# Kernel tuning notes

Measured on AMD Instinct MI355X. Metric: run time of the kernel, lower is better.

The kernel has to match this reference:

```python
import jax, jax.numpy as jnp
import numpy as np

N_NODES = 50000
N_EDGES = 800000
D_IN = 128
HIDDEN = 128
NUM_GRAPHS = 64
NUM_CLASSES = 6


def setup_inputs() -> dict:
    key = jax.random.key(0)
    ks = jax.random.split(key, 12)
    x = jax.random.normal(ks[0], (N_NODES, D_IN), dtype=jnp.float32)
    edge_index = jax.random.randint(ks[1], (2, N_EDGES), 0, N_NODES, dtype=jnp.int64)
    batch = jnp.sort(jax.random.randint(ks[2], (N_NODES,), 0, NUM_GRAPHS, dtype=jnp.int64))
    def glorot(k, fan_in, fan_out):
        s = jnp.sqrt(6.0 / (fan_in + fan_out)).astype(jnp.float32)
        return jax.random.uniform(k, (fan_in, fan_out), jnp.float32, -s, s)
    W0 = glorot(ks[3], D_IN, HIDDEN)
    b0 = jnp.zeros((HIDDEN,), jnp.float32)
    W1 = glorot(ks[4], HIDDEN, HIDDEN)
    b1 = jnp.zeros((HIDDEN,), jnp.float32)
    W2 = glorot(ks[5], HIDDEN, HIDDEN)
    b2 = jnp.zeros((HIDDEN,), jnp.float32)
    lin_W = glorot(ks[6], HIDDEN, NUM_CLASSES)
    lin_b = jnp.zeros((NUM_CLASSES,), jnp.float32)
    return {"x": x, "edge_index": edge_index, "batch": batch,
            "W0": W0, "b0": b0, "W1": W1, "b1": b1, "W2": W2, "b2": b2,
            "lin_W": lin_W, "lin_b": lin_b}


def reference(x, edge_index, batch, W0, b0, W1, b1, W2, b2, lin_W, lin_b):
    # GCNConv (PyG default): add self-loops, symmetric degree norm,
    # out = scatter_add(norm * (xW)[src] -> dst) + bias, then ReLU.
    loop = jnp.arange(N_NODES, dtype=edge_index.dtype)
    src = jnp.concatenate([edge_index[0], loop])  # message sources (x_j)
    dst = jnp.concatenate([edge_index[1], loop])  # aggregation targets
    deg = jax.ops.segment_sum(jnp.ones_like(dst, x.dtype), dst, num_segments=N_NODES)
    dinv = jnp.where(deg > 0, jax.lax.rsqrt(deg), 0.0)
    norm = (dinv[src] * dinv[dst])[:, None]  # [E+N, 1]

    h = x
    for W, b in ((W0, b0), (W1, b1), (W2, b2)):
        hw = h @ W                                   # [N, H] dense projection
        agg = jax.ops.segment_sum(hw[src] * norm, dst, num_segments=N_NODES)
        h = jax.nn.relu(agg + b)

    # global_mean_pool over graph ids
    counts = jax.ops.segment_sum(jnp.ones((N_NODES,), x.dtype), batch, num_segments=NUM_GRAPHS)
    embedding = jax.ops.segment_sum(h, batch, num_segments=NUM_GRAPHS) / jnp.maximum(counts, 1.0)[:, None]
    # dropout is identity in eval mode
    logits = embedding @ lin_W + lin_b
    return logits, embedding
```

## Files before the change

### kernel.cpp

```cpp
#include <hip/hip_runtime.h>

#define N_NODES 50000
#define HIDDEN 128
#define NUM_GRAPHS 64
#define NUM_CLASSES 6
#define SLOT_SHIFT 6
#define NB 392
#define BUCKET_CAP 3072
#define P1_CHUNK 2048
#define CONV_BLOCKS 192
#define LSTR 136

typedef __attribute__((ext_vector_type(8))) short short8;
typedef __attribute__((ext_vector_type(4))) float float4v;
typedef __attribute__((ext_vector_type(2))) float float2v;

__device__ __forceinline__ unsigned short f2b(float f) {
    unsigned u = __float_as_uint(f);
    return (unsigned short)((u + 0x7FFFu + ((u >> 16) & 1u)) >> 16);
}
__device__ __forceinline__ unsigned char f2e4m3(float f) {
    return (unsigned char)(__builtin_amdgcn_cvt_pk_fp8_f32(f, f, 0, false) & 0xFF);
}

__global__ __launch_bounds__(256) void pass1(const float* __restrict__ W0, const float* __restrict__ W1,
                                             const float* __restrict__ W2, unsigned short* __restrict__ wb,
                                             const int* __restrict__ src, const int* __restrict__ dst,
                                             int* __restrict__ gcursor, unsigned* __restrict__ ebuf, int e) {
    if (blockIdx.x < CONV_BLOCKS) {
        int i = blockIdx.x * 256 + threadIdx.x;
        int wsel = i >> 14;
        int r = i & 16383;
        int j = r & 7;
        int lane = (r >> 3) & 63;
        int f = r >> 9;
        int ki = f >> 3, nt = f & 7;
        int k = ki * 32 + (lane >> 4) * 8 + j;
        int c = nt * 16 + (lane & 15);
        const float* W = (wsel == 0) ? W0 : ((wsel == 1) ? W1 : W2);
        wb[i] = f2b(W[k * 128 + c]);
        return;
    }
    __shared__ unsigned hist[NB];
    __shared__ unsigned base[NB];
    const int t = threadIdx.x;
    const int start = (blockIdx.x - CONV_BLOCKS) * P1_CHUNK;
    for (int i = t; i < NB; i += 256) hist[i] = 0;
    __syncthreads();
    int lb[8];
    unsigned pk[8], lr[8];
#pragma unroll
    for (int k = 0; k < 8; k++) {
        int i = start + k * 256 + t;
        lb[k] = -1;
        if (i < e) {
            int d = dst[i];
            int s = src[i];
            lb[k] = d >> 7;
            pk[k] = ((unsigned)(d & 127) << 16) | (unsigned)s;
            lr[k] = atomicAdd(&hist[lb[k]], 1u);
        }
    }
    __syncthreads();
    for (int b = t; b < NB; b += 256)
        base[b] = (unsigned)atomicAdd(&gcursor[b], (int)hist[b]);
    __syncthreads();
#pragma unroll
    for (int k = 0; k < 8; k++) {
        if (lb[k] >= 0) {
            unsigned pos = base[lb[k]] + lr[k];
            if (pos < BUCKET_CAP) ebuf[lb[k] * BUCKET_CAP + pos] = pk[k];
        }
    }
}

__global__ __launch_bounds__(256) void pass2(const unsigned* __restrict__ ebuf, const int* __restrict__ gcursor,
                                             const float* __restrict__ x,
                                             unsigned short* __restrict__ csr16, int* __restrict__ cntc,
                                             float* __restrict__ dinv, unsigned char* __restrict__ xs8, int n) {
    __shared__ unsigned short csr_lds[128 * 64];
    __shared__ unsigned cnt[128];
    const int b = blockIdx.x;
    const int t = threadIdx.x;
    if (t < 128) {
        cnt[t] = 0;
        csr_lds[t * 64] = (unsigned short)(b * 128 + t);
    }
    __syncthreads();
    const int nb = min(gcursor[b], BUCKET_CAP);
    for (int i = t; i < nb; i += 256) {
        unsigned e = ebuf[b * BUCKET_CAP + i];
        int dl = (int)(e >> 16);
        unsigned r = atomicAdd(&cnt[dl], 1u);
        if (r < 63) csr_lds[dl * 64 + 1 + r] = (unsigned short)(e & 0xFFFFu);
    }
    __syncthreads();
    {
        const unsigned* cu = (const unsigned*)csr_lds;
        unsigned* gout = (unsigned*)(csr16 + (size_t)b * 8192);
#pragma unroll
        for (int it = 0; it < 16; it++) gout[it * 256 + t] = cu[it * 256 + t];
    }
    if (t < 128) {
        int node = b * 128 + t;
        if (node < n) {
            int deg1 = (int)cnt[t] + 1;
            cntc[node] = min(deg1, 64);
            dinv[node] = rsqrtf((float)deg1);
        }
    }
#pragma unroll
    for (int it = 0; it < 16; it++) {
        int idx = it * 256 + t;
        int nl = idx >> 5;
        int el = (idx & 31) * 4;
        int gnode = b * 128 + nl;
        if (gnode < n) {
            float sc = rsqrtf((float)((int)cnt[nl] + 1));
            float4 v = *(const float4*)&x[gnode * 128 + el];
            unsigned lo = __builtin_amdgcn_cvt_pk_fp8_f32(v.x * sc, v.y * sc, 0, false);
            unsigned pkd = __builtin_amdgcn_cvt_pk_fp8_f32(v.z * sc, v.w * sc, lo, true);
            *(unsigned*)&xs8[gnode * 128 + el] = pkd;
        }
    }
}

__global__ __launch_bounds__(256) void fused_layer(const unsigned char* __restrict__ hs8,
                                                   const int* __restrict__ cntc,
                                                   const unsigned short* __restrict__ csr16,
                                                   const float* __restrict__ dinv,
                                                   const unsigned short* __restrict__ wb,
                                                   const float* __restrict__ bias,
                                                   const float* __restrict__ rowscale,
                                                   unsigned char* __restrict__ hout8,
                                                   const int* __restrict__ batchp,
                                                   float* __restrict__ embp) {
    __shared__ __align__(16) unsigned short tlds[16 * LSTR];
    __shared__ int bsh[16];
    const int wave = threadIdx.x >> 6;
    const int lane = threadIdx.x & 63;
    const int grp = lane >> 4;
    const int fl = lane & 15;
    const int node0 = blockIdx.x * 16;
    const int base_node = node0 + wave * 4;

    int nbv[4], mycv[4];
#pragma unroll
    for (int i = 0; i < 4; i++) nbv[i] = cntc[base_node + i];
#pragma unroll
    for (int i = 0; i < 4; i++)
        mycv[i] = (lane < nbv[i]) ? (int)csr16[((base_node + i) << SLOT_SHIFT) + lane] : 0;

    for (int i = 0; i < 4; i++) {
        const int node = base_node + i;
        const int nb = nbv[i];
        const int nbm1 = nb - 1;
        float acc[8];
#pragma unroll
        for (int j = 0; j < 8; j++) acc[j] = 0.f;
        int myc = mycv[i];
        for (int c0 = 0; c0 < nb; c0 += 32) {
            int cc[8];
            float m[8];
#pragma unroll
            for (int k = 0; k < 8; k++) {
                int e = c0 + k * 4 + grp;
                m[k] = (e < nb) ? 1.f : 0.f;
                cc[k] = __shfl(myc, min(e, nbm1), 64);
            }
            uint2 u[8];
#pragma unroll
            for (int k = 0; k < 8; k++)
                u[k] = *(const uint2*)&hs8[cc[k] * 128 + fl * 8];
#pragma unroll
            for (int k = 0; k < 8; k++) {
                float2v f01 = __builtin_amdgcn_cvt_pk_f32_fp8(u[k].x, false);
                float2v f23 = __builtin_amdgcn_cvt_pk_f32_fp8(u[k].x, true);
                float2v f45 = __builtin_amdgcn_cvt_pk_f32_fp8(u[k].y, false);
                float2v f67 = __builtin_amdgcn_cvt_pk_f32_fp8(u[k].y, true);
                acc[0] += m[k] * f01.x;  acc[1] += m[k] * f01.y;
                acc[2] += m[k] * f23.x;  acc[3] += m[k] * f23.y;
                acc[4] += m[k] * f45.x;  acc[5] += m[k] * f45.y;
                acc[6] += m[k] * f67.x;  acc[7] += m[k] * f67.y;
            }
        }
#pragma unroll
        for (int j = 0; j < 8; j++) {
            acc[j] += __shfl_xor(acc[j], 16, 64);
            acc[j] += __shfl_xor(acc[j], 32, 64);
        }
        if (grp == 0) {
            const float dv = dinv[node];
            short8 o;
#pragma unroll
            for (int j = 0; j < 8; j++) o[j] = (short)f2b(acc[j] * dv);
            *(short8*)&tlds[(wave * 4 + i) * LSTR + fl * 8] = o;
        }
    }
    if (embp && threadIdx.x < 16) bsh[threadIdx.x] = batchp[node0 + threadIdx.x];
    __syncthreads();

    const int m = fl;
    const int quad = grp;
    const int nt0 = wave * 2;
    const short* B = (const short*)wb;
    float4v acc2[2];
    acc2[0] = (float4v){0.f, 0.f, 0.f, 0.f};
    acc2[1] = (float4v){0.f, 0.f, 0.f, 0.f};
#pragma unroll
    for (int ki = 0; ki < 4; ki++) {
        short8 a = *(const short8*)&tlds[m * LSTR + ki * 32 + quad * 8];
#pragma unroll
        for (int q = 0; q < 2; q++) {
            short8 b = *(const short8*)&B[((ki * 8 + nt0 + q) * 64 + lane) * 8];
            acc2[q] = __builtin_amdgcn_mfma_f32_16x16x32_bf16(a, b, acc2[q], 0, 0, 0);
        }
    }

    if (!embp) {
        float sc[4];
#pragma unroll
        for (int reg = 0; reg < 4; reg++) {
            int row = node0 + quad * 4 + reg;
            sc[reg] = rowscale[row];
        }
#pragma unroll
        for (int q = 0; q < 2; q++) {
            int c = (nt0 + q) * 16 + m;
            float bv = bias[c];
#pragma unroll
            for (int reg = 0; reg < 4; reg++) {
                int row = node0 + quad * 4 + reg;
                float v = fmaxf(acc2[q][reg] + bv, 0.f) * sc[reg];
                hout8[row * 128 + c] = f2e4m3(v);
            }
        }
    } else {
        const int g0 = bsh[0], g15 = bsh[15];
#pragma unroll
        for (int q = 0; q < 2; q++) {
            int c = (nt0 + q) * 16 + m;
            float bv = bias[c];
            float v0 = fmaxf(acc2[q][0] + bv, 0.f);
            float v1 = fmaxf(acc2[q][1] + bv, 0.f);
            float v2 = fmaxf(acc2[q][2] + bv, 0.f);
            float v3 = fmaxf(acc2[q][3] + bv, 0.f);
            if (g0 == g15) {
                float s = v0 + v1 + v2 + v3;
                s += __shfl_xor(s, 16, 64);
                s += __shfl_xor(s, 32, 64);
                if (quad == 0) atomicAdd(&embp[g0 * HIDDEN + c], s);
            } else {
                for (int gg = g0; gg <= g15; ++gg) {
                    float s = (bsh[quad * 4 + 0] == gg ? v0 : 0.f)
                            + (bsh[quad * 4 + 1] == gg ? v1 : 0.f)
                            + (bsh[quad * 4 + 2] == gg ? v2 : 0.f)
                            + (bsh[quad * 4 + 3] == gg ? v3 : 0.f);
                    s += __shfl_xor(s, 16, 64);
                    s += __shfl_xor(s, 32, 64);
                    if (quad == 0) atomicAdd(&embp[gg * HIDDEN + c], s);
                }
            }
        }
    }
}

__global__ __launch_bounds__(128) void finalize_kernel(const float* __restrict__ emb,
                                                       const int* __restrict__ batch,
                                                       const float* __restrict__ linW, const float* __restrict__ linb,
                                                       float* out, int n) {
    const int g = blockIdx.x;
    const int f = threadIdx.x;
    __shared__ float es[128];
    __shared__ int bnd[2];
    if (f < 2) {
        int target = g + f;
        int lo = 0, hi = n;
        while (lo < hi) {
            int mid = (lo + hi) >> 1;
            if (batch[mid] < target) lo = mid + 1; else hi = mid;
        }
        bnd[f] = lo;
    }
    __syncthreads();
    float c = (float)max(bnd[1] - bnd[0], 1);
    float e = emb[g * HIDDEN + f] / c;
    out[NUM_GRAPHS * NUM_CLASSES + g * HIDDEN + f] = e;
    es[f] = e;
    __syncthreads();
    if (f < NUM_CLASSES) {
        float s = linb[f];
        for (int k = 0; k < HIDDEN; k++) s += es[k] * linW[k * NUM_CLASSES + f];
        out[g * NUM_CLASSES + f] = s;
    }
}

extern "C" void kernel_launch(void* const* d_in, const int* in_sizes, int n_in,
                              void* d_out, int out_size, void* d_ws, size_t ws_size,
                              hipStream_t stream) {
    const float* x    = (const float*)d_in[0];
    const int*   ei   = (const int*)d_in[1];
    const int*   batch= (const int*)d_in[2];
    const float* W0   = (const float*)d_in[3];
    const float* b0   = (const float*)d_in[4];
    const float* W1   = (const float*)d_in[5];
    const float* b1   = (const float*)d_in[6];
    const float* W2   = (const float*)d_in[7];
    const float* b2   = (const float*)d_in[8];
    const float* linW = (const float*)d_in[9];
    const float* linb = (const float*)d_in[10];
    float* out = (float*)d_out;

    const int N = N_NODES;
    const int E = in_sizes[1] / 2;
    const int* srcp = ei;
    const int* dstp = ei + E;

    char* w = (char*)d_ws;
    size_t o = 0;
    auto alloc = [&](size_t bytes) { size_t r = o; o += (bytes + 255) & ~(size_t)255; return r; };
    int*            gcursor = (int*)           (w + alloc((size_t)NB * 4));
    float*          emb     = (float*)         (w + alloc((size_t)NUM_GRAPHS * HIDDEN * 4));
    size_t zero_bytes = o;
    unsigned*       ebuf    = (unsigned*)      (w + alloc((size_t)NB * BUCKET_CAP * 4));
    unsigned short* csr16   = (unsigned short*)(w + alloc((size_t)NB * 128 * 64 * 2));
    int*            cntc    = (int*)           (w + alloc((size_t)N * 4));
    float*          dinv    = (float*)         (w + alloc((size_t)N * 4));
    unsigned char*  xs8     = (unsigned char*) (w + alloc((size_t)(NB * 128) * HIDDEN));
    unsigned char*  h8a     = (unsigned char*) (w + alloc((size_t)(NB * 128) * HIDDEN));
    unsigned char*  h8b     = (unsigned char*) (w + alloc((size_t)(NB * 128) * HIDDEN));
    unsigned short* wb      = (unsigned short*)(w + alloc((size_t)3 * 16384 * 2));

    hipMemsetAsync(d_ws, 0, zero_bytes, stream);

    const int p1_edge_blocks = (E + P1_CHUNK - 1) / P1_CHUNK;

    pass1<<<CONV_BLOCKS + p1_edge_blocks, 256, 0, stream>>>(W0, W1, W2, wb, srcp, dstp, gcursor, ebuf, E);
    pass2<<<NB, 256, 0, stream>>>(ebuf, gcursor, x, csr16, cntc, dinv, xs8, N);

    const int fuse_grid = N / 16;

    fused_layer<<<fuse_grid, 256, 0, stream>>>(xs8, cntc, csr16, dinv, wb + 0 * 16384, b0, dinv, h8a, nullptr, nullptr);
    fused_layer<<<fuse_grid, 256, 0, stream>>>(h8a, cntc, csr16, dinv, wb + 1 * 16384, b1, dinv, h8b, nullptr, nullptr);
    fused_layer<<<fuse_grid, 256, 0, stream>>>(h8b, cntc, csr16, dinv, wb + 2 * 16384, b2, nullptr, nullptr, batch, emb);

    finalize_kernel<<<NUM_GRAPHS, 128, 0, stream>>>(emb, batch, linW, linb, out, N);
}
```

Baseline: 223.4 us.

## Merge all kernels into one cooperative persistent kernel with grid syncs

Replaces the six separate launches (two preprocessing passes, three GCN layers, finalize) with one cooperative kernel. The kernel loops persistently over work items and separates phases with grid.sync(), which removes per-launch overhead and launch gaps. The neighbor-gather loop is also restructured to process full groups of 16 neighbors without masks, with a masked tail only for the final partial group, using packed float2 accumulators. The tradeoffs are fewer resident blocks per phase and the cost of grid-wide barriers, and the grid size assumes 256 CUs.

```diff
diff --git a/kernel.cpp b/kernel.cpp
--- a/kernel.cpp
+++ b/kernel.cpp
@@ -1,4 +1,7 @@
 #include <hip/hip_runtime.h>
+#include <hip/hip_cooperative_groups.h>
+
+namespace cg = cooperative_groups;
 
 #define N_NODES 50000
 #define HIDDEN 128
@@ -8,8 +11,9 @@
 #define NB 392
 #define BUCKET_CAP 3072
 #define P1_CHUNK 2048
-#define CONV_BLOCKS 192
+#define CONV_CHUNKS 192
 #define LSTR 136
+#define TILES (N_NODES / 16)
 
 typedef __attribute__((ext_vector_type(8))) short short8;
 typedef __attribute__((ext_vector_type(4))) float float4v;
@@ -23,275 +27,310 @@
     return (unsigned char)(__builtin_amdgcn_cvt_pk_fp8_f32(f, f, 0, false) & 0xFF);
 }
 
-__global__ __launch_bounds__(256) void pass1(const float* __restrict__ W0, const float* __restrict__ W1,
-                                             const float* __restrict__ W2, unsigned short* __restrict__ wb,
-                                             const int* __restrict__ src, const int* __restrict__ dst,
-                                             int* __restrict__ gcursor, unsigned* __restrict__ ebuf, int e) {
-    if (blockIdx.x < CONV_BLOCKS) {
-        int i = blockIdx.x * 256 + threadIdx.x;
-        int wsel = i >> 14;
-        int r = i & 16383;
-        int j = r & 7;
-        int lane = (r >> 3) & 63;
-        int f = r >> 9;
-        int ki = f >> 3, nt = f & 7;
-        int k = ki * 32 + (lane >> 4) * 8 + j;
-        int c = nt * 16 + (lane & 15);
-        const float* W = (wsel == 0) ? W0 : ((wsel == 1) ? W1 : W2);
-        wb[i] = f2b(W[k * 128 + c]);
-        return;
-    }
-    __shared__ unsigned hist[NB];
-    __shared__ unsigned base[NB];
-    const int t = threadIdx.x;
-    const int start = (blockIdx.x - CONV_BLOCKS) * P1_CHUNK;
-    for (int i = t; i < NB; i += 256) hist[i] = 0;
-    __syncthreads();
-    int lb[8];
-    unsigned pk[8], lr[8];
-#pragma unroll
-    for (int k = 0; k < 8; k++) {
-        int i = start + k * 256 + t;
-        lb[k] = -1;
-        if (i < e) {
-            int d = dst[i];
-            int s = src[i];
-            lb[k] = d >> 7;
-            pk[k] = ((unsigned)(d & 127) << 16) | (unsigned)s;
-            lr[k] = atomicAdd(&hist[lb[k]], 1u);
-        }
-    }
-    __syncthreads();
-    for (int b = t; b < NB; b += 256)
-        base[b] = (unsigned)atomicAdd(&gcursor[b], (int)hist[b]);
-    __syncthreads();
-#pragma unroll
-    for (int k = 0; k < 8; k++) {
-        if (lb[k] >= 0) {
-            unsigned pos = base[lb[k]] + lr[k];
-            if (pos < BUCKET_CAP) ebuf[lb[k] * BUCKET_CAP + pos] = pk[k];
-        }
-    }
-}
-
-__global__ __launch_bounds__(256) void pass2(const unsigned* __restrict__ ebuf, const int* __restrict__ gcursor,
-                                             const float* __restrict__ x,
-                                             unsigned short* __restrict__ csr16, int* __restrict__ cntc,
-                                             float* __restrict__ dinv, unsigned char* __restrict__ xs8, int n) {
-    __shared__ unsigned short csr_lds[128 * 64];
-    __shared__ unsigned cnt[128];
-    const int b = blockIdx.x;
-    const int t = threadIdx.x;
-    if (t < 128) {
-        cnt[t] = 0;
-        csr_lds[t * 64] = (unsigned short)(b * 128 + t);
-    }
-    __syncthreads();
-    const int nb = min(gcursor[b], BUCKET_CAP);
-    for (int i = t; i < nb; i += 256) {
-        unsigned e = ebuf[b * BUCKET_CAP + i];
-        int dl = (int)(e >> 16);
-        unsigned r = atomicAdd(&cnt[dl], 1u);
-        if (r < 63) csr_lds[dl * 64 + 1 + r] = (unsigned short)(e & 0xFFFFu);
-    }
-    __syncthreads();
-    {
-        const unsigned* cu = (const unsigned*)csr_lds;
-        unsigned* gout = (unsigned*)(csr16 + (size_t)b * 8192);
-#pragma unroll
-        for (int it = 0; it < 16; it++) gout[it * 256 + t] = cu[it * 256 + t];
-    }
-    if (t < 128) {
-        int node = b * 128 + t;
-        if (node < n) {
-            int deg1 = (int)cnt[t] + 1;
-            cntc[node] = min(deg1, 64);
-            dinv[node] = rsqrtf((float)deg1);
-        }
-    }
-#pragma unroll
-    for (int it = 0; it < 16; it++) {
-        int idx = it * 256 + t;
-        int nl = idx >> 5;
-        int el = (idx & 31) * 4;
-        int gnode = b * 128 + nl;
-        if (gnode < n) {
-            float sc = rsqrtf((float)((int)cnt[nl] + 1));
-            float4 v = *(const float4*)&x[gnode * 128 + el];
-            unsigned lo = __builtin_amdgcn_cvt_pk_fp8_f32(v.x * sc, v.y * sc, 0, false);
-            unsigned pkd = __builtin_amdgcn_cvt_pk_fp8_f32(v.z * sc, v.w * sc, lo, true);
-            *(unsigned*)&xs8[gnode * 128 + el] = pkd;
-        }
-    }
-}
-
-__global__ __launch_bounds__(256) void fused_layer(const unsigned char* __restrict__ hs8,
-                                                   const int* __restrict__ cntc,
-                                                   const unsigned short* __restrict__ csr16,
-                                                   const float* __restrict__ dinv,
-                                                   const unsigned short* __restrict__ wb,
-                                                   const float* __restrict__ bias,
-                                                   const float* __restrict__ rowscale,
-                                                   unsigned char* __restrict__ hout8,
-                                                   const int* __restrict__ batchp,
-                                                   float* __restrict__ embp) {
-    __shared__ __align__(16) unsigned short tlds[16 * LSTR];
-    __shared__ int bsh[16];
+struct MegaArgs {
+    const float* x;
+    const int* src; const int* dst; const int* batch;
+    const float* W0; const float* b0; const float* W1; const float* b1;
+    const float* W2; const float* b2; const float* linW; const float* linb;
+    float* out;
+    int* gcursor; float* emb;
+    unsigned* ebuf; unsigned short* csr16; int* cntc; float* dinv;
+    unsigned char* xs8; unsigned char* h8a; unsigned char* h8b;
+    unsigned short* wb;
+    int E; int nec;
+};
+
+template <bool LAST>
+__device__ void layer_phase(const MegaArgs& A, const unsigned char* __restrict__ hin,
+                            const unsigned short* __restrict__ wbp,
+                            const float* __restrict__ bias,
+                            unsigned char* __restrict__ hout,
+                            unsigned char* smem, int gsz) {
+    unsigned short* tlds = (unsigned short*)smem;
+    int* bsh = (int*)(smem + 16 * LSTR * 2);
     const int wave = threadIdx.x >> 6;
     const int lane = threadIdx.x & 63;
     const int grp = lane >> 4;
     const int fl = lane & 15;
-    const int node0 = blockIdx.x * 16;
-    const int base_node = node0 + wave * 4;
-
-    int nbv[4], mycv[4];
-#pragma unroll
-    for (int i = 0; i < 4; i++) nbv[i] = cntc[base_node + i];
-#pragma unroll
-    for (int i = 0; i < 4; i++)
-        mycv[i] = (lane < nbv[i]) ? (int)csr16[((base_node + i) << SLOT_SHIFT) + lane] : 0;
-
-    for (int i = 0; i < 4; i++) {
-        const int node = base_node + i;
-        const int nb = nbv[i];
-        const int nbm1 = nb - 1;
-        float acc[8];
-#pragma unroll
-        for (int j = 0; j < 8; j++) acc[j] = 0.f;
-        int myc = mycv[i];
-        for (int c0 = 0; c0 < nb; c0 += 32) {
-            int cc[8];
-            float m[8];
-#pragma unroll
-            for (int k = 0; k < 8; k++) {
-                int e = c0 + k * 4 + grp;
-                m[k] = (e < nb) ? 1.f : 0.f;
-                cc[k] = __shfl(myc, min(e, nbm1), 64);
-            }
-            uint2 u[8];
-#pragma unroll
-            for (int k = 0; k < 8; k++)
-                u[k] = *(const uint2*)&hs8[cc[k] * 128 + fl * 8];
-#pragma unroll
-            for (int k = 0; k < 8; k++) {
-                float2v f01 = __builtin_amdgcn_cvt_pk_f32_fp8(u[k].x, false);
-                float2v f23 = __builtin_amdgcn_cvt_pk_f32_fp8(u[k].x, true);
-                float2v f45 = __builtin_amdgcn_cvt_pk_f32_fp8(u[k].y, false);
-                float2v f67 = __builtin_amdgcn_cvt_pk_f32_fp8(u[k].y, true);
-                acc[0] += m[k] * f01.x;  acc[1] += m[k] * f01.y;
-                acc[2] += m[k] * f23.x;  acc[3] += m[k] * f23.y;
-                acc[4] += m[k] * f45.x;  acc[5] += m[k] * f45.y;
-                acc[6] += m[k] * f67.x;  acc[7] += m[k] * f67.y;
-            }
-        }
-#pragma unroll
-        for (int j = 0; j < 8; j++) {
-            acc[j] += __shfl_xor(acc[j], 16, 64);
-            acc[j] += __shfl_xor(acc[j], 32, 64);
-        }
-        if (grp == 0) {
-            const float dv = dinv[node];
-            short8 o;
-#pragma unroll
-            for (int j = 0; j < 8; j++) o[j] = (short)f2b(acc[j] * dv);
-            *(short8*)&tlds[(wave * 4 + i) * LSTR + fl * 8] = o;
-        }
-    }
-    if (embp && threadIdx.x < 16) bsh[threadIdx.x] = batchp[node0 + threadIdx.x];
-    __syncthreads();
-
-    const int m = fl;
-    const int quad = grp;
-    const int nt0 = wave * 2;
-    const short* B = (const short*)wb;
-    float4v acc2[2];
-    acc2[0] = (float4v){0.f, 0.f, 0.f, 0.f};
-    acc2[1] = (float4v){0.f, 0.f, 0.f, 0.f};
-#pragma unroll
-    for (int ki = 0; ki < 4; ki++) {
-        short8 a = *(const short8*)&tlds[m * LSTR + ki * 32 + quad * 8];
-#pragma unroll
-        for (int q = 0; q < 2; q++) {
-            short8 b = *(const short8*)&B[((ki * 8 + nt0 + q) * 64 + lane) * 8];
-            acc2[q] = __builtin_amdgcn_mfma_f32_16x16x32_bf16(a, b, acc2[q], 0, 0, 0);
-        }
-    }
-
-    if (!embp) {
-        float sc[4];
-#pragma unroll
-        for (int reg = 0; reg < 4; reg++) {
-            int row = node0 + quad * 4 + reg;
-            sc[reg] = rowscale[row];
-        }
-#pragma unroll
-        for (int q = 0; q < 2; q++) {
-            int c = (nt0 + q) * 16 + m;
-            float bv = bias[c];
-#pragma unroll
-            for (int reg = 0; reg < 4; reg++) {
-                int row = node0 + quad * 4 + reg;
-                float v = fmaxf(acc2[q][reg] + bv, 0.f) * sc[reg];
-                hout8[row * 128 + c] = f2e4m3(v);
-            }
-        }
-    } else {
-        const int g0 = bsh[0], g15 = bsh[15];
-#pragma unroll
-        for (int q = 0; q < 2; q++) {
-            int c = (nt0 + q) * 16 + m;
-            float bv = bias[c];
-            float v0 = fmaxf(acc2[q][0] + bv, 0.f);
-            float v1 = fmaxf(acc2[q][1] + bv, 0.f);
-            float v2 = fmaxf(acc2[q][2] + bv, 0.f);
-            float v3 = fmaxf(acc2[q][3] + bv, 0.f);
-            if (g0 == g15) {
-                float s = v0 + v1 + v2 + v3;
-                s += __shfl_xor(s, 16, 64);
-                s += __shfl_xor(s, 32, 64);
-                if (quad == 0) atomicAdd(&embp[g0 * HIDDEN + c], s);
-            } else {
-                for (int gg = g0; gg <= g15; ++gg) {
-                    float s = (bsh[quad * 4 + 0] == gg ? v0 : 0.f)
-                            + (bsh[quad * 4 + 1] == gg ? v1 : 0.f)
-                            + (bsh[quad * 4 + 2] == gg ? v2 : 0.f)
-                            + (bsh[quad * 4 + 3] == gg ? v3 : 0.f);
+
+    for (int tile = blockIdx.x; tile < TILES; tile += gsz) {
+        const int node0 = tile * 16;
+        const int base_node = node0 + wave * 4;
+
+        int nbv[4], mycv[4];
+#pragma unroll
+        for (int i = 0; i < 4; i++) nbv[i] = A.cntc[base_node + i];
+#pragma unroll
+        for (int i = 0; i < 4; i++)
+            mycv[i] = (lane < nbv[i]) ? (int)A.csr16[((base_node + i) << SLOT_SHIFT) + lane] : 0;
+
+        for (int i = 0; i < 4; i++) {
+            const int node = base_node + i;
+            const int nb = nbv[i];
+            const int myc = mycv[i];
+            float2v a01 = {0.f, 0.f}, a23 = {0.f, 0.f}, a45 = {0.f, 0.f}, a67 = {0.f, 0.f};
+
+            const int nh = nb >> 4;
+            for (int h = 0; h < nh; h++) {
+                const int base = h << 4;
+                int cc[4];
+#pragma unroll
+                for (int k = 0; k < 4; k++) cc[k] = __shfl(myc, base + k * 4 + grp, 64);
+                uint2 u[4];
+#pragma unroll
+                for (int k = 0; k < 4; k++) u[k] = *(const uint2*)&hin[cc[k] * 128 + fl * 8];
+#pragma unroll
+                for (int k = 0; k < 4; k++) {
+                    a01 += __builtin_amdgcn_cvt_pk_f32_fp8(u[k].x, false);
+                    a23 += __builtin_amdgcn_cvt_pk_f32_fp8(u[k].x, true);
+                    a45 += __builtin_amdgcn_cvt_pk_f32_fp8(u[k].y, false);
+                    a67 += __builtin_amdgcn_cvt_pk_f32_fp8(u[k].y, true);
+                }
+            }
+            const int rem = (nb >> 2) & 3;
+            const int rbase = nh << 4;
+            for (int r = 0; r < rem; r++) {
+                int cc = __shfl(myc, rbase + r * 4 + grp, 64);
+                uint2 u = *(const uint2*)&hin[cc * 128 + fl * 8];
+                a01 += __builtin_amdgcn_cvt_pk_f32_fp8(u.x, false);
+                a23 += __builtin_amdgcn_cvt_pk_f32_fp8(u.x, true);
+                a45 += __builtin_amdgcn_cvt_pk_f32_fp8(u.y, false);
+                a67 += __builtin_amdgcn_cvt_pk_f32_fp8(u.y, true);
+            }
+            if (nb & 3) {
+                int e = (nb & ~3) + grp;
+                float mmv = (e < nb) ? 1.f : 0.f;
+                int cc = __shfl(myc, min(e, nb - 1), 64);
+                uint2 u = *(const uint2*)&hin[cc * 128 + fl * 8];
+                float2v m2 = {mmv, mmv};
+                a01 += m2 * __builtin_amdgcn_cvt_pk_f32_fp8(u.x, false);
+                a23 += m2 * __builtin_amdgcn_cvt_pk_f32_fp8(u.x, true);
+                a45 += m2 * __builtin_amdgcn_cvt_pk_f32_fp8(u.y, false);
+                a67 += m2 * __builtin_amdgcn_cvt_pk_f32_fp8(u.y, true);
+            }
+
+            float acc[8] = {a01.x, a01.y, a23.x, a23.y, a45.x, a45.y, a67.x, a67.y};
+#pragma unroll
+            for (int j = 0; j < 8; j++) {
+                acc[j] += __shfl_xor(acc[j], 16, 64);
+                acc[j] += __shfl_xor(acc[j], 32, 64);
+            }
+            if (grp == 0) {
+                const float dv = A.dinv[node];
+                short8 o;
+#pragma unroll
+                for (int j = 0; j < 8; j++) o[j] = (short)f2b(acc[j] * dv);
+                *(short8*)&tlds[(wave * 4 + i) * LSTR + fl * 8] = o;
+            }
+        }
+        if (LAST && threadIdx.x < 16) bsh[threadIdx.x] = A.batch[node0 + threadIdx.x];
+        __syncthreads();
+
+        const int m = fl;
+        const int quad = grp;
+        const int nt0 = wave * 2;
+        const short* B = (const short*)wbp;
+        float4v acc2[2];
+        acc2[0] = (float4v){0.f, 0.f, 0.f, 0.f};
+        acc2[1] = (float4v){0.f, 0.f, 0.f, 0.f};
+#pragma unroll
+        for (int ki = 0; ki < 4; ki++) {
+            short8 a = *(const short8*)&tlds[m * LSTR + ki * 32 + quad * 8];
+#pragma unroll
+            for (int q = 0; q < 2; q++) {
+                short8 b = *(const short8*)&B[((ki * 8 + nt0 + q) * 64 + lane) * 8];
+                acc2[q] = __builtin_amdgcn_mfma_f32_16x16x32_bf16(a, b, acc2[q], 0, 0, 0);
+            }
+        }
+
+        if (!LAST) {
+            float sc[4];
+#pragma unroll
+            for (int reg = 0; reg < 4; reg++) sc[reg] = A.dinv[node0 + quad * 4 + reg];
+#pragma unroll
+            for (int q = 0; q < 2; q++) {
+                int c = (nt0 + q) * 16 + m;
+                float bv = bias[c];
+#pragma unroll
+                for (int reg = 0; reg < 4; reg++) {
+                    int row = node0 + quad * 4 + reg;
+                    float v = fmaxf(acc2[q][reg] + bv, 0.f) * sc[reg];
+                    hout[row * 128 + c] = f2e4m3(v);
+                }
+            }
+        } else {
+            const int g0 = bsh[0], g15 = bsh[15];
+#pragma unroll
+            for (int q = 0; q < 2; q++) {
+                int c = (nt0 + q) * 16 + m;
+                float bv = bias[c];
+                float v0 = fmaxf(acc2[q][0] + bv, 0.f);
+                float v1 = fmaxf(acc2[q][1] + bv, 0.f);
+                float v2 = fmaxf(acc2[q][2] + bv, 0.f);
+                float v3 = fmaxf(acc2[q][3] + bv, 0.f);
+                if (g0 == g15) {
+                    float s = v0 + v1 + v2 + v3;
                     s += __shfl_xor(s, 16, 64);
                     s += __shfl_xor(s, 32, 64);
-                    if (quad == 0) atomicAdd(&embp[gg * HIDDEN + c], s);
-                }
-            }
-        }
+                    if (quad == 0) atomicAdd(&A.emb[g0 * HIDDEN + c], s);
+                } else {
+                    for (int gg = g0; gg <= g15; ++gg) {
+                        float s = (bsh[quad * 4 + 0] == gg ? v0 : 0.f)
+                                + (bsh[quad * 4 + 1] == gg ? v1 : 0.f)
+                                + (bsh[quad * 4 + 2] == gg ? v2 : 0.f)
+                                + (bsh[quad * 4 + 3] == gg ? v3 : 0.f);
+                        s += __shfl_xor(s, 16, 64);
+                        s += __shfl_xor(s, 32, 64);
+                        if (quad == 0) atomicAdd(&A.emb[gg * HIDDEN + c], s);
+                    }
+                }
+            }
+        }
+        __syncthreads();
     }
 }
 
-__global__ __launch_bounds__(128) void finalize_kernel(const float* __restrict__ emb,
-                                                       const int* __restrict__ batch,
-                                                       const float* __restrict__ linW, const float* __restrict__ linb,
-                                                       float* out, int n) {
-    const int g = blockIdx.x;
-    const int f = threadIdx.x;
-    __shared__ float es[128];
-    __shared__ int bnd[2];
-    if (f < 2) {
-        int target = g + f;
-        int lo = 0, hi = n;
-        while (lo < hi) {
-            int mid = (lo + hi) >> 1;
-            if (batch[mid] < target) lo = mid + 1; else hi = mid;
-        }
-        bnd[f] = lo;
+__global__ __launch_bounds__(256, 4) void mega(MegaArgs A) {
+    __shared__ __align__(16) unsigned char smem[16896];
+    cg::grid_group grid = cg::this_grid();
+    const int t = threadIdx.x;
+    const int gsz = gridDim.x;
+
+    {
+        unsigned* hist = (unsigned*)smem;
+        unsigned* hbase = hist + NB;
+        const int nwork = CONV_CHUNKS + A.nec;
+        for (int w = blockIdx.x; w < nwork; w += gsz) {
+            if (w < CONV_CHUNKS) {
+                int i = w * 256 + t;
+                int wsel = i >> 14;
+                int r = i & 16383;
+                int j = r & 7;
+                int lane = (r >> 3) & 63;
+                int f = r >> 9;
+                int ki = f >> 3, nt = f & 7;
+                int k = ki * 32 + (lane >> 4) * 8 + j;
+                int c = nt * 16 + (lane & 15);
+                const float* W = (wsel == 0) ? A.W0 : ((wsel == 1) ? A.W1 : A.W2);
+                A.wb[i] = f2b(W[k * 128 + c]);
+            } else {
+                const int start = (w - CONV_CHUNKS) * P1_CHUNK;
+                for (int i = t; i < NB; i += 256) hist[i] = 0;
+                __syncthreads();
+                int lb[8];
+                unsigned pk[8], lr[8];
+#pragma unroll
+                for (int k = 0; k < 8; k++) {
+                    int i = start + k * 256 + t;
+                    lb[k] = -1;
+                    if (i < A.E) {
+                        int d = A.dst[i];
+                        int s = A.src[i];
+                        lb[k] = d >> 7;
+                        pk[k] = ((unsigned)(d & 127) << 16) | (unsigned)s;
+                        lr[k] = atomicAdd(&hist[lb[k]], 1u);
+                    }
+                }
+                __syncthreads();
+                for (int b = t; b < NB; b += 256)
+                    hbase[b] = (unsigned)atomicAdd(&A.gcursor[b], (int)hist[b]);
+                __syncthreads();
+#pragma unroll
+                for (int k = 0; k < 8; k++) {
+                    if (lb[k] >= 0) {
+                        unsigned pos = hbase[lb[k]] + lr[k];
+                        if (pos < BUCKET_CAP) A.ebuf[lb[k] * BUCKET_CAP + pos] = pk[k];
+                    }
+                }
+                __syncthreads();
+            }
+        }
     }
-    __syncthreads();
-    float c = (float)max(bnd[1] - bnd[0], 1);
-    float e = emb[g * HIDDEN + f] / c;
-    out[NUM_GRAPHS * NUM_CLASSES + g * HIDDEN + f] = e;
-    es[f] = e;
-    __syncthreads();
-    if (f < NUM_CLASSES) {
-        float s = linb[f];
-        for (int k = 0; k < HIDDEN; k++) s += es[k] * linW[k * NUM_CLASSES + f];
-        out[g * NUM_CLASSES + f] = s;
+    grid.sync();
+
+    {
+        unsigned short* csr_lds = (unsigned short*)smem;
+        unsigned* cnt = (unsigned*)(smem + 16384);
+        for (int b = blockIdx.x; b < NB; b += gsz) {
+            if (t < 128) {
+                cnt[t] = 0;
+                csr_lds[t * 64] = (unsigned short)(b * 128 + t);
+            }
+            __syncthreads();
+            const int nb = min(A.gcursor[b], BUCKET_CAP);
+            for (int i = t; i < nb; i += 256) {
+                unsigned e = A.ebuf[b * BUCKET_CAP + i];
+                int dl = (int)(e >> 16);
+                unsigned r = atomicAdd(&cnt[dl], 1u);
+                if (r < 63) csr_lds[dl * 64 + 1 + r] = (unsigned short)(e & 0xFFFFu);
+            }
+            __syncthreads();
+            {
+                const unsigned* cu = (const unsigned*)csr_lds;
+                unsigned* gout = (unsigned*)(A.csr16 + (size_t)b * 8192);
+#pragma unroll
+                for (int it = 0; it < 16; it++) gout[it * 256 + t] = cu[it * 256 + t];
+            }
+            if (t < 128) {
+                int node = b * 128 + t;
+                if (node < N_NODES) {
+                    int deg1 = (int)cnt[t] + 1;
+                    A.cntc[node] = min(deg1, 64);
+                    A.dinv[node] = rsqrtf((float)deg1);
+                }
+            }
+#pragma unroll
+            for (int it = 0; it < 16; it++) {
+                int idx = it * 256 + t;
+                int nl = idx >> 5;
+                int el = (idx & 31) * 4;
+                int gnode = b * 128 + nl;
+                if (gnode < N_NODES) {
+                    float sc = rsqrtf((float)((int)cnt[nl] + 1));
+                    float4 v = *(const float4*)&A.x[gnode * 128 + el];
+                    unsigned lo = __builtin_amdgcn_cvt_pk_fp8_f32(v.x * sc, v.y * sc, 0, false);
+                    unsigned pkd = __builtin_amdgcn_cvt_pk_fp8_f32(v.z * sc, v.w * sc, lo, true);
+                    *(unsigned*)&A.xs8[gnode * 128 + el] = pkd;
+                }
+            }
+            __syncthreads();
+        }
+    }
+    grid.sync();
+
+    layer_phase<false>(A, A.xs8, A.wb,         A.b0, A.h8a, smem, gsz);
+    grid.sync();
+    layer_phase<false>(A, A.h8a, A.wb + 16384, A.b1, A.h8b, smem, gsz);
+    grid.sync();
+    layer_phase<true >(A, A.h8b, A.wb + 32768, A.b2, nullptr, smem, gsz);
+    grid.sync();
+
+    if (blockIdx.x < NUM_GRAPHS) {
+        float* es = (float*)smem;
+        int* bnd = (int*)(smem + 512);
+        const int g = blockIdx.x;
+        if (t < 2) {
+            int target = g + t;
+            int lo = 0, hi = N_NODES;
+            while (lo < hi) {
+                int mid = (lo + hi) >> 1;
+                if (A.batch[mid] < target) lo = mid + 1; else hi = mid;
+            }
+            bnd[t] = lo;
+        }
+        __syncthreads();
+        if (t < 128) {
+            float c = (float)max(bnd[1] - bnd[0], 1);
+            float e = A.emb[g * HIDDEN + t] / c;
+            A.out[NUM_GRAPHS * NUM_CLASSES + g * HIDDEN + t] = e;
+            es[t] = e;
+        }
+        __syncthreads();
+        if (t < NUM_CLASSES) {
+            float s = A.linb[t];
+            for (int k = 0; k < HIDDEN; k++) s += es[k] * A.linW[k * NUM_CLASSES + t];
+            A.out[g * NUM_CLASSES + t] = s;
+        }
     }
 }
 
@@ -301,20 +340,9 @@
     const float* x    = (const float*)d_in[0];
     const int*   ei   = (const int*)d_in[1];
     const int*   batch= (const int*)d_in[2];
-    const float* W0   = (const float*)d_in[3];
-    const float* b0   = (const float*)d_in[4];
-    const float* W1   = (const float*)d_in[5];
-    const float* b1   = (const float*)d_in[6];
-    const float* W2   = (const float*)d_in[7];
-    const float* b2   = (const float*)d_in[8];
-    const float* linW = (const float*)d_in[9];
-    const float* linb = (const float*)d_in[10];
-    float* out = (float*)d_out;
 
     const int N = N_NODES;
     const int E = in_sizes[1] / 2;
-    const int* srcp = ei;
-    const int* dstp = ei + E;
 
     char* w = (char*)d_ws;
     size_t o = 0;
@@ -333,16 +361,24 @@
 
     hipMemsetAsync(d_ws, 0, zero_bytes, stream);
 
-    const int p1_edge_blocks = (E + P1_CHUNK - 1) / P1_CHUNK;
-
-    pass1<<<CONV_BLOCKS + p1_edge_blocks, 256, 0, stream>>>(W0, W1, W2, wb, srcp, dstp, gcursor, ebuf, E);
-    pass2<<<NB, 256, 0, stream>>>(ebuf, gcursor, x, csr16, cntc, dinv, xs8, N);
-
-    const int fuse_grid = N / 16;
-
-    fused_layer<<<fuse_grid, 256, 0, stream>>>(xs8, cntc, csr16, dinv, wb + 0 * 16384, b0, dinv, h8a, nullptr, nullptr);
-    fused_layer<<<fuse_grid, 256, 0, stream>>>(h8a, cntc, csr16, dinv, wb + 1 * 16384, b1, dinv, h8b, nullptr, nullptr);
-    fused_layer<<<fuse_grid, 256, 0, stream>>>(h8b, cntc, csr16, dinv, wb + 2 * 16384, b2, nullptr, nullptr, batch, emb);
-
-    finalize_kernel<<<NUM_GRAPHS, 128, 0, stream>>>(emb, batch, linW, linb, out, N);
-}
+    MegaArgs ha;
+    ha.x = x; ha.src = ei; ha.dst = ei + E; ha.batch = batch;
+    ha.W0 = (const float*)d_in[3]; ha.b0 = (const float*)d_in[4];
+    ha.W1 = (const float*)d_in[5]; ha.b1 = (const float*)d_in[6];
+    ha.W2 = (const float*)d_in[7]; ha.b2 = (const float*)d_in[8];
+    ha.linW = (const float*)d_in[9]; ha.linb = (const float*)d_in[10];
+    ha.out = (float*)d_out;
+    ha.gcursor = gcursor; ha.emb = emb;
+    ha.ebuf = ebuf; ha.csr16 = csr16; ha.cntc = cntc; ha.dinv = dinv;
+    ha.xs8 = xs8; ha.h8a = h8a; ha.h8b = h8b; ha.wb = wb;
+    ha.E = E; ha.nec = (E + P1_CHUNK - 1) / P1_CHUNK;
+
+    int nblk = 0;
+    hipError_t oe = hipOccupancyMaxActiveBlocksPerMultiprocessor(&nblk, (const void*)mega, 256, 0);
+    if (oe != hipSuccess || nblk < 1) nblk = 4;
+    int grid = nblk * 256;
+    if (grid > 2048) grid = 2048;
+
+    void* params[] = { (void*)&ha };
+    hipLaunchCooperativeKernel((const void*)mega, dim3(grid), dim3(256), params, 0, stream);
+}
```

Result: slower. 614.0 us (+174.9%).
